# Optimization experiments

Hardware: AMD Instinct MI355X
Metric: run time of the kernel (lower is better)

Reference implementation:

```python
import jax, jax.numpy as jnp
import numpy as np

V, DM, DEPTH, N = 50257, 512, 8, 16  # vocab, dim, depth, ssm_dim
B, L = 2, 1024
GATE = 0.5  # fixed_gate=True blend


def layer_norm(x, g, b):
    mu = x.mean(-1, keepdims=True)
    xm = x - mu
    var = (xm * xm).mean(-1, keepdims=True)
    return xm * jax.lax.rsqrt(var + 1e-5) * g + b


def ssm(u, W_dt, b_dt, W_B, W_C, A_log, D_p):
    # selective SSM: h_t = exp(dt_t*A)*h_{t-1} + dt_t*B_t*u_t ; y_t = C_t.h_t + D*u_t
    dt = jax.nn.softplus(u @ W_dt + b_dt)            # (B,L,DM)
    Bm = u @ W_B                                      # (B,L,N)
    Cm = u @ W_C                                      # (B,L,N)
    A = -jnp.exp(A_log)                               # (DM,N), stable (negative)

    def step(h, inp):
        dt_t, B_t, C_t, u_t = inp                     # (B,DM),(B,N),(B,N),(B,DM)
        h = jnp.exp(dt_t[..., None] * A) * h + (dt_t * u_t)[..., None] * B_t[:, None, :]
        y = jnp.einsum('bdn,bn->bd', h, C_t)
        return h, y

    h0 = jnp.zeros((u.shape[0], DM, N), u.dtype)
    xs = (dt.transpose(1, 0, 2), Bm.transpose(1, 0, 2), Cm.transpose(1, 0, 2), u.transpose(1, 0, 2))
    _, ys = jax.lax.scan(step, h0, xs)
    return ys.transpose(1, 0, 2) + D_p * u


def wkv(x, W_r, W_k, W_v, W_o, t_decay, t_first):
    # RWKV-4 channel-wise WKV recurrence
    r = jax.nn.sigmoid(x @ W_r)
    k = jnp.clip(x @ W_k, -30.0, 30.0)
    v = x @ W_v
    w = jnp.exp(-jnp.exp(t_decay))                    # (DM,) decay in (0,1)

    def step(carry, inp):
        a, b = carry
        k_t, v_t = inp
        ek = jnp.exp(k_t)
        eu = jnp.exp(t_first + k_t)
        out = (a + eu * v_t) / (b + eu + 1e-6)
        return (w * a + ek * v_t, w * b + ek), out

    a0 = jnp.zeros((x.shape[0], DM), x.dtype)
    _, o = jax.lax.scan(step, (a0, jnp.zeros_like(a0)), (k.transpose(1, 0, 2), v.transpose(1, 0, 2)))
    return (r * o.transpose(1, 0, 2)) @ W_o


def setup_inputs() -> dict:
    key = jax.random.key(0)
    ks = jax.random.split(key, 16)
    s = 0.02
    inp = {
        'input_ids': jax.random.randint(ks[0], (B, L), 0, V, dtype=jnp.int32),
        'emb': jax.random.normal(ks[1], (V, DM), jnp.float32) * s,
        'ln1_g': jnp.ones((DEPTH, DM), jnp.float32),
        'ln1_b': jnp.zeros((DEPTH, DM), jnp.float32),
        'W_dt': jax.random.normal(ks[2], (DEPTH, DM, DM), jnp.float32) * s,
        'b_dt': jnp.zeros((DEPTH, DM), jnp.float32),
        'W_B': jax.random.normal(ks[3], (DEPTH, DM, N), jnp.float32) * s,
        'W_C': jax.random.normal(ks[4], (DEPTH, DM, N), jnp.float32) * s,
        'A_log': jnp.broadcast_to(jnp.log(jnp.arange(1, N + 1, dtype=jnp.float32)), (DEPTH, DM, N)).copy(),
        'D_p': jnp.ones((DEPTH, DM), jnp.float32),
        'ln2_g': jnp.ones((DEPTH, DM), jnp.float32),
        'ln2_b': jnp.zeros((DEPTH, DM), jnp.float32),
        'W_r': jax.random.normal(ks[5], (DEPTH, DM, DM), jnp.float32) * s,
        'W_k': jax.random.normal(ks[6], (DEPTH, DM, DM), jnp.float32) * s,
        'W_v': jax.random.normal(ks[7], (DEPTH, DM, DM), jnp.float32) * s,
        'W_o': jax.random.normal(ks[8], (DEPTH, DM, DM), jnp.float32) * s,
        't_decay': jax.random.normal(ks[9], (DEPTH, DM), jnp.float32) * 0.5,
        't_first': jax.random.normal(ks[10], (DEPTH, DM), jnp.float32) * 0.5,
        'lnf_g': jnp.ones((DM,), jnp.float32),
        'lnf_b': jnp.zeros((DM,), jnp.float32),
    }
    return inp


def reference(input_ids, emb, ln1_g, ln1_b, W_dt, b_dt, W_B, W_C, A_log, D_p,
              ln2_g, ln2_b, W_r, W_k, W_v, W_o, t_decay, t_first, lnf_g, lnf_b):
    x = emb[input_ids]                                # (B,L,DM)
    for i in range(DEPTH):
        x = x + GATE * ssm(layer_norm(x, ln1_g[i], ln1_b[i]),
                           W_dt[i], b_dt[i], W_B[i], W_C[i], A_log[i], D_p[i])
        x = x + GATE * wkv(layer_norm(x, ln2_g[i], ln2_b[i]),
                           W_r[i], W_k[i], W_v[i], W_o[i], t_decay[i], t_first[i])
    x = layer_norm(x, lnf_g, lnf_b)
    logits = x @ emb.T                                # tied LM head, (B,L,V)
    return logits
```

## Files before the change

kernel.cpp:

```cpp
#include <hip/hip_runtime.h>

#define DM 512
#define NST 16
#define NDEPTH 8
#define NB 2
#define NL 1024
#define MROWS 2048
#define VOCAB 50257
#define VPAD  50304
#define NCH 32
#define CLEN 32

typedef __attribute__((ext_vector_type(8))) short bf16x8;
typedef __attribute__((ext_vector_type(4))) float f32x4;
typedef __attribute__((ext_vector_type(8))) unsigned short ushort8;

#define AS1(p) ((const __attribute__((address_space(1))) void*)(p))
#define AS3(p) ((__attribute__((address_space(3))) void*)(p))

static __device__ __forceinline__ unsigned short f2bf(float f) {
  unsigned int x = __float_as_uint(f);
  unsigned int r = (x + 0x7FFFu + ((x >> 16) & 1u)) >> 16;
  return (unsigned short)r;
}
static __device__ __forceinline__ float bf2f(unsigned short u) {
  return __uint_as_float((unsigned int)u << 16);
}

__global__ __launch_bounds__(256) void k_gather(const int* __restrict__ ids,
    const float* __restrict__ emb, float* __restrict__ x)
{
  int gid = blockIdx.x * 256 + threadIdx.x;
  int row = gid >> 7, c = (gid & 127) * 4;
  int id = ids[row];
  *(float4*)(x + (size_t)row * DM + c) = *(const float4*)(emb + (size_t)id * DM + c);
}

__global__ void k_transpose(const float* __restrict__ Wdt, const float* __restrict__ Wr,
    const float* __restrict__ Wk, const float* __restrict__ Wv, const float* __restrict__ Wo,
    unsigned short* __restrict__ Tdtbc, unsigned short* __restrict__ Trkv, unsigned short* __restrict__ To)
{
  __shared__ float tile[32][33];
  int z = blockIdx.z, layer = z / 5, f = z % 5;
  const float* src;
  unsigned short* dst;
  size_t lw = (size_t)layer * DM * DM;
  if (f == 0)      { src = Wdt + lw; dst = Tdtbc + (size_t)layer * 640 * DM; }
  else if (f == 1) { src = Wr  + lw; dst = Trkv + (size_t)layer * 3 * DM * DM; }
  else if (f == 2) { src = Wk  + lw; dst = Trkv + (size_t)layer * 3 * DM * DM + DM * DM; }
  else if (f == 3) { src = Wv  + lw; dst = Trkv + (size_t)layer * 3 * DM * DM + 2 * DM * DM; }
  else             { src = Wo  + lw; dst = To   + lw; }
  int tx = threadIdx.x, ty = threadIdx.y;
  int kb = blockIdx.y * 32, nb = blockIdx.x * 32;
  #pragma unroll
  for (int i = 0; i < 4; i++)
    tile[ty + i * 8][tx] = src[(size_t)(kb + ty + i * 8) * DM + nb + tx];
  __syncthreads();
  #pragma unroll
  for (int i = 0; i < 4; i++)
    dst[(size_t)(nb + ty + i * 8) * DM + kb + tx] = f2bf(tile[tx][ty + i * 8]);
}

__global__ __launch_bounds__(256) void k_bcpack(const float* __restrict__ WB,
    const float* __restrict__ WC, unsigned short* __restrict__ Tdtbc)
{
  int gid = blockIdx.x * 256 + threadIdx.x;
  int k = gid & 511, n = (gid >> 9) & 127, layer = gid >> 16;
  float v = 0.f;
  if (n < 16)      v = WB[((size_t)layer * DM + k) * NST + n];
  else if (n < 32) v = WC[((size_t)layer * DM + k) * NST + (n - 16)];
  Tdtbc[(size_t)layer * 640 * DM + (size_t)(512 + n) * DM + k] = f2bf(v);
}

__global__ __launch_bounds__(256) void k_embcvt(const float* __restrict__ emb,
    unsigned short* __restrict__ out)
{
  int gid = blockIdx.x * 256 + threadIdx.x;
  size_t base = (size_t)gid * 8;
  int row = (int)(base >> 9);
  ushort8 o;
  if (row < VOCAB) {
    float4 a = *(const float4*)(emb + base);
    float4 b = *(const float4*)(emb + base + 4);
    o[0]=f2bf(a.x); o[1]=f2bf(a.y); o[2]=f2bf(a.z); o[3]=f2bf(a.w);
    o[4]=f2bf(b.x); o[5]=f2bf(b.y); o[6]=f2bf(b.z); o[7]=f2bf(b.w);
  } else {
    o = (ushort8)0;
  }
  *(ushort8*)(out + base) = o;
}

__global__ __launch_bounds__(256) void k_ln(const float* __restrict__ x,
    const float* __restrict__ g, const float* __restrict__ bb,
    float* __restrict__ of, unsigned short* __restrict__ ob)
{
  const int w = threadIdx.x >> 6, l = threadIdx.x & 63;
  const int row = blockIdx.x * 4 + w;
  const float* xr = x + (size_t)row * DM + l * 8;
  float4 v0 = *(const float4*)(xr);
  float4 v1 = *(const float4*)(xr + 4);
  float s = v0.x + v0.y + v0.z + v0.w + v1.x + v1.y + v1.z + v1.w;
  float q = v0.x*v0.x + v0.y*v0.y + v0.z*v0.z + v0.w*v0.w
          + v1.x*v1.x + v1.y*v1.y + v1.z*v1.z + v1.w*v1.w;
  #pragma unroll
  for (int m = 1; m < 64; m <<= 1) { s += __shfl_xor(s, m); q += __shfl_xor(q, m); }
  const float mu = s * (1.0f / DM);
  const float var = q * (1.0f / DM) - mu * mu;
  const float rs = rsqrtf(var + 1e-5f);
  const float4 g0 = *(const float4*)(g + l * 8);
  const float4 g1 = *(const float4*)(g + l * 8 + 4);
  const float4 b0 = *(const float4*)(bb + l * 8);
  const float4 b1 = *(const float4*)(bb + l * 8 + 4);
  float y[8];
  y[0] = (v0.x - mu) * rs * g0.x + b0.x;
  y[1] = (v0.y - mu) * rs * g0.y + b0.y;
  y[2] = (v0.z - mu) * rs * g0.z + b0.z;
  y[3] = (v0.w - mu) * rs * g0.w + b0.w;
  y[4] = (v1.x - mu) * rs * g1.x + b1.x;
  y[5] = (v1.y - mu) * rs * g1.y + b1.y;
  y[6] = (v1.z - mu) * rs * g1.z + b1.z;
  y[7] = (v1.w - mu) * rs * g1.w + b1.w;
  if (of) {
    float4 o0 = {y[0], y[1], y[2], y[3]}, o1 = {y[4], y[5], y[6], y[7]};
    *(float4*)(of + (size_t)row * DM + l * 8) = o0;
    *(float4*)(of + (size_t)row * DM + l * 8 + 4) = o1;
  }
  if (ob) {
    ushort8 o;
    #pragma unroll
    for (int j = 0; j < 8; j++) o[j] = f2bf(y[j]);
    *(ushort8*)(ob + (size_t)row * DM + l * 8) = o;
  }
}

template<int BM, int BN, int EPI>
__global__ __launch_bounds__(256) void gemm_bt(const unsigned short* __restrict__ A,
    const unsigned short* __restrict__ Bt, float* __restrict__ C, int N, int ldc,
    const float* __restrict__ bias, float* __restrict__ C2)
{
  constexpr int K = DM;
  constexpr int MI = BM / 32, NI = BN / 32;
  __shared__ unsigned short lsA[BM * 64];
  __shared__ unsigned short lsB[BN * 64];
  const int t = threadIdx.x;
  const int w = t >> 6, l = t & 63;
  const int wm = (w >> 1) * (BM / 2), wn = (w & 1) * (BN / 2);
  const size_t bm = (size_t)blockIdx.x * BM, bn = (size_t)blockIdx.y * BN;
  f32x4 acc[MI][NI] = {};
  const int srow = t >> 3, sslot = t & 7;
  const int gs = sslot ^ (srow & 7);
  const unsigned short* Ag = A + (bm + srow) * K + gs * 8;
  const unsigned short* Bg = Bt + (bn + srow) * K + gs * 8;
  const int lr = l & 15, lq = l >> 4;
  for (int k0 = 0; k0 < K; k0 += 64) {
    #pragma unroll
    for (int o = 0; o < BM / 32; ++o)
      __builtin_amdgcn_global_load_lds(AS1(Ag + (size_t)(o * 32) * K + k0),
          AS3(lsA + (o * 32 + srow) * 64 + sslot * 8), 16, 0, 0);
    #pragma unroll
    for (int o = 0; o < BN / 32; ++o)
      __builtin_amdgcn_global_load_lds(AS1(Bg + (size_t)(o * 32) * K + k0),
          AS3(lsB + (o * 32 + srow) * 64 + sslot * 8), 16, 0, 0);
    asm volatile("s_waitcnt vmcnt(0)" ::: "memory");
    __syncthreads();
    bf16x8 af[MI][2], bfr[NI][2];
    #pragma unroll
    for (int i = 0; i < MI; ++i) {
      int row = wm + i * 16 + lr;
      #pragma unroll
      for (int h = 0; h < 2; ++h)
        af[i][h] = *(const bf16x8*)(lsA + row * 64 + (((h * 4 + lq) ^ (row & 7)) * 8));
    }
    #pragma unroll
    for (int i = 0; i < NI; ++i) {
      int row = wn + i * 16 + lr;
      #pragma unroll
      for (int h = 0; h < 2; ++h)
        bfr[i][h] = *(const bf16x8*)(lsB + row * 64 + (((h * 4 + lq) ^ (row & 7)) * 8));
    }
    #pragma unroll
    for (int h = 0; h < 2; ++h)
      #pragma unroll
      for (int mi = 0; mi < MI; ++mi)
        #pragma unroll
        for (int ni = 0; ni < NI; ++ni)
          acc[mi][ni] = __builtin_amdgcn_mfma_f32_16x16x32_bf16(af[mi][h], bfr[ni][h], acc[mi][ni], 0, 0, 0);
    __syncthreads();
  }
  const int lg = l >> 4;
  #pragma unroll
  for (int mi = 0; mi < MI; ++mi) {
    #pragma unroll
    for (int ni = 0; ni < NI; ++ni) {
      int n = (int)bn + wn + ni * 16 + lr;
      size_t m0 = bm + wm + mi * 16 + lg * 4;
      #pragma unroll
      for (int j = 0; j < 4; ++j) {
        float v = acc[mi][ni][j];
        if (EPI == 0) {
          C[(m0 + j) * (size_t)ldc + n] = v;
        } else if (EPI == 2) {
          C2[(m0 + j) * (size_t)ldc + n] += 0.5f * v;
        } else {
          if (n < 512) {
            float b = v + bias[n];
            C[(m0 + j) * (size_t)512 + n] = fmaxf(b, 0.f) + log1pf(__expf(-fabsf(b)));
          } else if (n < 544) {
            C2[(m0 + j) * (size_t)32 + (n - 512)] = v;
          }
        }
      }
    }
  }
}

__global__ __launch_bounds__(512) void gemm_head(const unsigned short* __restrict__ A,
    const unsigned short* __restrict__ Bt, float* __restrict__ C)
{
  __shared__ unsigned short lsA[256 * 64];
  __shared__ unsigned short lsB[128 * 64];
  const int t = threadIdx.x;
  const int w = t >> 6, l = t & 63;
  const int wm = (w >> 1) * 64, wn = (w & 1) * 64;
  const int c = (int)blockIdx.x & 7, j = (int)blockIdx.x >> 3;
  const int ntile = c * 50 + (j >> 3), mtile = j & 7;
  if (ntile >= 393) return;
  const size_t bm = (size_t)mtile * 256, bn = (size_t)ntile * 128;
  f32x4 acc[4][4] = {};
  const int srow = t >> 3, sslot = t & 7;
  const int gs = sslot ^ (srow & 7);
  const unsigned short* Ag = A + (bm + srow) * DM + gs * 8;
  const unsigned short* Bg = Bt + (bn + srow) * DM + gs * 8;
  const int lr = l & 15, lq = l >> 4;
  for (int k0 = 0; k0 < DM; k0 += 64) {
    #pragma unroll
    for (int o = 0; o < 4; ++o)
      __builtin_amdgcn_global_load_lds(AS1(Ag + (size_t)(o * 64) * DM + k0),
          AS3(lsA + (o * 64 + srow) * 64 + sslot * 8), 16, 0, 0);
    #pragma unroll
    for (int o = 0; o < 2; ++o)
      __builtin_amdgcn_global_load_lds(AS1(Bg + (size_t)(o * 64) * DM + k0),
          AS3(lsB + (o * 64 + srow) * 64 + sslot * 8), 16, 0, 0);
    asm volatile("s_waitcnt vmcnt(0)" ::: "memory");
    __syncthreads();
    bf16x8 af[4][2], bfr[4][2];
    #pragma unroll
    for (int i = 0; i < 4; ++i) {
      int row = wm + i * 16 + lr;
      #pragma unroll
      for (int h = 0; h < 2; ++h)
        af[i][h] = *(const bf16x8*)(lsA + row * 64 + (((h * 4 + lq) ^ (row & 7)) * 8));
    }
    #pragma unroll
    for (int i = 0; i < 4; ++i) {
      int row = wn + i * 16 + lr;
      #pragma unroll
      for (int h = 0; h < 2; ++h)
        bfr[i][h] = *(const bf16x8*)(lsB + row * 64 + (((h * 4 + lq) ^ (row & 7)) * 8));
    }
    #pragma unroll
    for (int h = 0; h < 2; ++h)
      #pragma unroll
      for (int mi = 0; mi < 4; ++mi)
        #pragma unroll
        for (int ni = 0; ni < 4; ++ni)
          acc[mi][ni] = __builtin_amdgcn_mfma_f32_16x16x32_bf16(af[mi][h], bfr[ni][h], acc[mi][ni], 0, 0, 0);
    __syncthreads();
  }
  const int lg = l >> 4;
  #pragma unroll
  for (int mi = 0; mi < 4; ++mi) {
    #pragma unroll
    for (int ni = 0; ni < 4; ++ni) {
      int n = (int)bn + wn + ni * 16 + lr;
      if (n >= VOCAB) continue;
      size_t m0 = bm + wm + mi * 16 + lg * 4;
      #pragma unroll
      for (int jj = 0; jj < 4; ++jj)
        C[(m0 + jj) * (size_t)VOCAB + n] = acc[mi][ni][jj];
    }
  }
}

__global__ __launch_bounds__(256) void k_ssm1(const float* __restrict__ dt,
    const unsigned short* __restrict__ u, const float* __restrict__ BC,
    const float* __restrict__ A_log, float* __restrict__ Pb, float* __restrict__ Sb)
{
  const int t = threadIdx.x;
  const int grp = t >> 4, n = t & 15;
  const int cg = blockIdx.x & 63, ck = blockIdx.x >> 6;
  const int ch = cg * 16 + grp;
  const int b = ch >> 9, d = ch & 511;
  const float A = -__expf(A_log[d * NST + n]);
  const int t0 = ck * CLEN;
  const float* dtp = dt + ((size_t)b * NL + t0) * DM + d;
  const unsigned short* up = u + ((size_t)b * NL + t0) * DM + d;
  const float* bcp = BC + ((size_t)b * NL + t0) * 32 + n;
  float P = 1.f, S = 0.f;
  #pragma unroll
  for (int tt = 0; tt < CLEN; ++tt) {
    float dtv = dtp[(size_t)tt * DM];
    float uv  = bf2f(up[(size_t)tt * DM]);
    float Bv  = bcp[(size_t)tt * 32];
    float e = __expf(dtv * A);
    S = fmaf(e, S, dtv * uv * Bv);
    P *= e;
  }
  size_t cn = (size_t)ch * NST + n;
  Pb[cn * NCH + ck] = P;
  Sb[cn * NCH + ck] = S;
}

__global__ __launch_bounds__(256) void k_ssm2(const float* __restrict__ Pb,
    const float* __restrict__ Sb, float* __restrict__ H0)
{
  const int wid = blockIdx.x * 8 + (threadIdx.x >> 5);
  const int lane = threadIdx.x & 31;
  float coef = Pb[(size_t)wid * NCH + lane];
  float sum  = Sb[(size_t)wid * NCH + lane];
  #pragma unroll
  for (int m = 1; m < 32; m <<= 1) {
    float cr = __shfl_up(coef, m, 32);
    float sr = __shfl_up(sum, m, 32);
    if (lane >= m) { sum = fmaf(coef, sr, sum); coef *= cr; }
  }
  float hp = __shfl_up(sum, 1, 32);
  H0[(size_t)wid * NCH + lane] = (lane == 0) ? 0.f : hp;
}

__global__ __launch_bounds__(256) void k_ssm3(const float* __restrict__ dt,
    const unsigned short* __restrict__ u, const float* __restrict__ BC,
    const float* __restrict__ A_log, const float* __restrict__ Dp,
    const float* __restrict__ H0, float* __restrict__ x)
{
  const int t = threadIdx.x;
  const int grp = t >> 4, n = t & 15;
  const int cg = blockIdx.x & 63, ck = blockIdx.x >> 6;
  const int ch = cg * 16 + grp;
  const int b = ch >> 9, d = ch & 511;
  const float A = -__expf(A_log[d * NST + n]);
  const float Dpv = Dp[d];
  const int t0 = ck * CLEN;
  const float* dtp = dt + ((size_t)b * NL + t0) * DM + d;
  const unsigned short* up = u + ((size_t)b * NL + t0) * DM + d;
  const float* bcp = BC + ((size_t)b * NL + t0) * 32 + n;
  float* xp = x + ((size_t)b * NL + t0) * DM + d;
  size_t cn = (size_t)ch * NST + n;
  float h = H0[cn * NCH + ck];
  #pragma unroll
  for (int tt = 0; tt < CLEN; ++tt) {
    float dtv = dtp[(size_t)tt * DM];
    float uv  = bf2f(up[(size_t)tt * DM]);
    float Bv  = bcp[(size_t)tt * 32];
    float Cv  = bcp[(size_t)tt * 32 + 16];
    float e = __expf(dtv * A);
    h = fmaf(e, h, dtv * uv * Bv);
    float p2 = h * Cv;
    p2 += __shfl_xor(p2, 1);
    p2 += __shfl_xor(p2, 2);
    p2 += __shfl_xor(p2, 4);
    p2 += __shfl_xor(p2, 8);
    if (n == 0) xp[(size_t)tt * DM] += 0.5f * (p2 + Dpv * uv);
  }
}

__global__ __launch_bounds__(256) void k_wkv1(const float* __restrict__ rkv,
    const float* __restrict__ tdec, float* __restrict__ SaB, float* __restrict__ SbB)
{
  const int gid = blockIdx.x * 256 + threadIdx.x;
  const int ch = gid & 1023, ck = gid >> 10;
  const int b = ch >> 9, d = ch & 511;
  const float w = __expf(-__expf(tdec[d]));
  const float* base = rkv + ((size_t)b * NL + ck * CLEN) * 1536;
  float Sa = 0.f, Sb = 0.f;
  #pragma unroll
  for (int tt = 0; tt < CLEN; ++tt) {
    const float* row = base + (size_t)tt * 1536;
    float kt = row[512 + d];
    kt = fminf(30.f, fmaxf(-30.f, kt));
    float vt = row[1024 + d];
    float ek = __expf(kt);
    Sa = fmaf(w, Sa, ek * vt);
    Sb = fmaf(w, Sb, ek);
  }
  SaB[(size_t)ch * NCH + ck] = Sa;
  SbB[(size_t)ch * NCH + ck] = Sb;
}

__global__ __launch_bounds__(256) void k_wkv2(const float* __restrict__ SaB,
    const float* __restrict__ SbB, const float* __restrict__ tdec,
    float* __restrict__ HaB, float* __restrict__ HbB)
{
  const int ch = blockIdx.x * 8 + (threadIdx.x >> 5);
  const int lane = threadIdx.x & 31;
  const int d = ch & 511;
  float coef = __expf(-32.f * __expf(tdec[d]));
  float sa = SaB[(size_t)ch * NCH + lane];
  float sb = SbB[(size_t)ch * NCH + lane];
  #pragma unroll
  for (int m = 1; m < 32; m <<= 1) {
    float cr  = __shfl_up(coef, m, 32);
    float sar = __shfl_up(sa, m, 32);
    float sbr = __shfl_up(sb, m, 32);
    if (lane >= m) { sa = fmaf(coef, sar, sa); sb = fmaf(coef, sbr, sb); coef *= cr; }
  }
  float ha = __shfl_up(sa, 1, 32);
  float hb = __shfl_up(sb, 1, 32);
  HaB[(size_t)ch * NCH + lane] = (lane == 0) ? 0.f : ha;
  HbB[(size_t)ch * NCH + lane] = (lane == 0) ? 0.f : hb;
}

__global__ __launch_bounds__(256) void k_wkv3(const float* __restrict__ rkv,
    const float* __restrict__ tdec, const float* __restrict__ tfir,
    const float* __restrict__ HaB, const float* __restrict__ HbB,
    unsigned short* __restrict__ ro)
{
  const int gid = blockIdx.x * 256 + threadIdx.x;
  const int ch = gid & 1023, ck = gid >> 10;
  const int b = ch >> 9, d = ch & 511;
  const float w = __expf(-__expf(tdec[d]));
  const float tf = tfir[d];
  float a = HaB[(size_t)ch * NCH + ck];
  float bden = HbB[(size_t)ch * NCH + ck];
  const int t0 = ck * CLEN;
  const float* base = rkv + ((size_t)b * NL + t0) * 1536;
  unsigned short* rop = ro + ((size_t)b * NL + t0) * DM + d;
  #pragma unroll
  for (int tt = 0; tt < CLEN; ++tt) {
    const float* row = base + (size_t)tt * 1536;
    float rv = row[d];
    float kt = row[512 + d];
    kt = fminf(30.f, fmaxf(-30.f, kt));
    float vt = row[1024 + d];
    float ek = __expf(kt);
    float eu = __expf(tf + kt);
    float out = __fdividef(a + eu * vt, bden + eu + 1e-6f);
    float sig = __fdividef(1.f, 1.f + __expf(-rv));
    rop[(size_t)tt * DM] = f2bf(sig * out);
    a = fmaf(w, a, ek * vt);
    bden = fmaf(w, bden, ek);
  }
}

extern "C" void kernel_launch(void* const* d_in, const int* in_sizes, int n_in,
                              void* d_out, int out_size, void* d_ws, size_t ws_size,
                              hipStream_t stream)
{
  const int*   ids   = (const int*)d_in[0];
  const float* emb   = (const float*)d_in[1];
  const float* ln1_g = (const float*)d_in[2];
  const float* ln1_b = (const float*)d_in[3];
  const float* W_dt  = (const float*)d_in[4];
  const float* b_dt  = (const float*)d_in[5];
  const float* W_B   = (const float*)d_in[6];
  const float* W_C   = (const float*)d_in[7];
  const float* A_log = (const float*)d_in[8];
  const float* D_p   = (const float*)d_in[9];
  const float* ln2_g = (const float*)d_in[10];
  const float* ln2_b = (const float*)d_in[11];
  const float* W_r   = (const float*)d_in[12];
  const float* W_k   = (const float*)d_in[13];
  const float* W_v   = (const float*)d_in[14];
  const float* W_o   = (const float*)d_in[15];
  const float* t_dec = (const float*)d_in[16];
  const float* t_fir = (const float*)d_in[17];
  const float* lnf_g = (const float*)d_in[18];
  const float* lnf_b = (const float*)d_in[19];

  char* p = (char*)d_ws;
  float*          xres  = (float*)(p + 0);
  float*          dtb   = (float*)(p + 8388608);
  float*          rkv   = (float*)(p + 12582912);
  float*          BCb   = (float*)(p + 25165824);
  unsigned short* abuf  = (unsigned short*)(p + 25427968);
  unsigned short* Tdtbc = (unsigned short*)(p + 27525120);
  unsigned short* To    = (unsigned short*)(p + 32768000);
  unsigned short* Trkv  = (unsigned short*)(p + 36962304);
  unsigned short* Tem   = (unsigned short*)(p + 49545216);

  float* Pb  = rkv;
  float* Sb  = rkv + 524288;
  float* H0  = rkv + 1048576;
  float* SaB = dtb;
  float* SbB = dtb + 32768;
  float* HaB = dtb + 65536;
  float* HbB = dtb + 98304;

  k_gather<<<1024, 256, 0, stream>>>(ids, emb, xres);
  k_transpose<<<dim3(16, 16, 40), dim3(32, 8), 0, stream>>>(W_dt, W_r, W_k, W_v, W_o, Tdtbc, Trkv, To);
  k_bcpack<<<2048, 256, 0, stream>>>(W_B, W_C, Tdtbc);
  k_embcvt<<<12576, 256, 0, stream>>>(emb, Tem);

  for (int i = 0; i < NDEPTH; ++i) {
    k_ln<<<512, 256, 0, stream>>>(xres, ln1_g + i * DM, ln1_b + i * DM, nullptr, abuf);
    gemm_bt<64, 128, 3><<<dim3(32, 5), 256, 0, stream>>>(abuf,
        Tdtbc + (size_t)i * 640 * DM, dtb, 640, 512, b_dt + i * DM, BCb);
    k_ssm1<<<2048, 256, 0, stream>>>(dtb, abuf, BCb, A_log + (size_t)i * DM * NST, Pb, Sb);
    k_ssm2<<<2048, 256, 0, stream>>>(Pb, Sb, H0);
    k_ssm3<<<2048, 256, 0, stream>>>(dtb, abuf, BCb, A_log + (size_t)i * DM * NST,
        D_p + i * DM, H0, xres);
    k_ln<<<512, 256, 0, stream>>>(xres, ln2_g + i * DM, ln2_b + i * DM, nullptr, abuf);
    gemm_bt<64, 128, 0><<<dim3(32, 12), 256, 0, stream>>>(abuf,
        Trkv + (size_t)i * 3 * DM * DM, rkv, 1536, 1536, nullptr, nullptr);
    k_wkv1<<<128, 256, 0, stream>>>(rkv, t_dec + i * DM, SaB, SbB);
    k_wkv2<<<128, 256, 0, stream>>>(SaB, SbB, t_dec + i * DM, HaB, HbB);
    k_wkv3<<<128, 256, 0, stream>>>(rkv, t_dec + i * DM, t_fir + i * DM, HaB, HbB, abuf);
    gemm_bt<64, 128, 2><<<dim3(32, 4), 256, 0, stream>>>(abuf,
        To + (size_t)i * DM * DM, nullptr, 512, 512, nullptr, xres);
  }

  k_ln<<<512, 256, 0, stream>>>(xres, lnf_g, lnf_b, nullptr, abuf);
  gemm_head<<<3200, 512, 0, stream>>>(abuf, Tem, (float*)d_out);
}
```

Before: 1.124 ms.

## Fuse three-phase SSM and WKV chunked scans into cooperative kernels with grid sync

Merges the three SSM scan kernels (chunk reduce, cross-chunk prefix, chunk apply) into one cooperative kernel, and does the same for the three WKV kernels. Phases are separated by grid-wide barriers instead of separate kernel launches. The SSM kernel runs on 1024 blocks, each handling two virtual blocks, so the whole grid can be resident at once. This removes launch gaps and per-launch overhead, at the cost of grid-sync latency and the residency constraint a cooperative launch imposes.

After: 3.606 ms. +220.7%, slower.

```diff
diff --git a/kernel.cpp b/kernel.cpp
--- a/kernel.cpp
+++ b/kernel.cpp
@@ -1,4 +1,7 @@
 #include <hip/hip_runtime.h>
+#include <hip/hip_cooperative_groups.h>
+
+namespace cg = cooperative_groups;
 
 #define DM 512
 #define NST 16
@@ -282,163 +285,158 @@
   }
 }
 
-__global__ __launch_bounds__(256) void k_ssm1(const float* __restrict__ dt,
+__global__ __launch_bounds__(256, 4) void k_ssm_all(const float* __restrict__ dt,
     const unsigned short* __restrict__ u, const float* __restrict__ BC,
-    const float* __restrict__ A_log, float* __restrict__ Pb, float* __restrict__ Sb)
-{
+    const float* __restrict__ A_log, const float* __restrict__ Dp,
+    float* __restrict__ Pb, float* __restrict__ Sb, float* __restrict__ H0,
+    float* __restrict__ x)
+{
+  cg::grid_group gridg = cg::this_grid();
   const int t = threadIdx.x;
   const int grp = t >> 4, n = t & 15;
-  const int cg = blockIdx.x & 63, ck = blockIdx.x >> 6;
-  const int ch = cg * 16 + grp;
-  const int b = ch >> 9, d = ch & 511;
-  const float A = -__expf(A_log[d * NST + n]);
-  const int t0 = ck * CLEN;
-  const float* dtp = dt + ((size_t)b * NL + t0) * DM + d;
-  const unsigned short* up = u + ((size_t)b * NL + t0) * DM + d;
-  const float* bcp = BC + ((size_t)b * NL + t0) * 32 + n;
-  float P = 1.f, S = 0.f;
-  #pragma unroll
-  for (int tt = 0; tt < CLEN; ++tt) {
-    float dtv = dtp[(size_t)tt * DM];
-    float uv  = bf2f(up[(size_t)tt * DM]);
-    float Bv  = bcp[(size_t)tt * 32];
-    float e = __expf(dtv * A);
-    S = fmaf(e, S, dtv * uv * Bv);
-    P *= e;
-  }
-  size_t cn = (size_t)ch * NST + n;
-  Pb[cn * NCH + ck] = P;
-  Sb[cn * NCH + ck] = S;
-}
-
-__global__ __launch_bounds__(256) void k_ssm2(const float* __restrict__ Pb,
-    const float* __restrict__ Sb, float* __restrict__ H0)
-{
-  const int wid = blockIdx.x * 8 + (threadIdx.x >> 5);
-  const int lane = threadIdx.x & 31;
-  float coef = Pb[(size_t)wid * NCH + lane];
-  float sum  = Sb[(size_t)wid * NCH + lane];
-  #pragma unroll
-  for (int m = 1; m < 32; m <<= 1) {
-    float cr = __shfl_up(coef, m, 32);
-    float sr = __shfl_up(sum, m, 32);
-    if (lane >= m) { sum = fmaf(coef, sr, sum); coef *= cr; }
-  }
-  float hp = __shfl_up(sum, 1, 32);
-  H0[(size_t)wid * NCH + lane] = (lane == 0) ? 0.f : hp;
-}
-
-__global__ __launch_bounds__(256) void k_ssm3(const float* __restrict__ dt,
-    const unsigned short* __restrict__ u, const float* __restrict__ BC,
-    const float* __restrict__ A_log, const float* __restrict__ Dp,
-    const float* __restrict__ H0, float* __restrict__ x)
-{
-  const int t = threadIdx.x;
-  const int grp = t >> 4, n = t & 15;
-  const int cg = blockIdx.x & 63, ck = blockIdx.x >> 6;
-  const int ch = cg * 16 + grp;
-  const int b = ch >> 9, d = ch & 511;
-  const float A = -__expf(A_log[d * NST + n]);
-  const float Dpv = Dp[d];
-  const int t0 = ck * CLEN;
-  const float* dtp = dt + ((size_t)b * NL + t0) * DM + d;
-  const unsigned short* up = u + ((size_t)b * NL + t0) * DM + d;
-  const float* bcp = BC + ((size_t)b * NL + t0) * 32 + n;
-  float* xp = x + ((size_t)b * NL + t0) * DM + d;
-  size_t cn = (size_t)ch * NST + n;
-  float h = H0[cn * NCH + ck];
-  #pragma unroll
-  for (int tt = 0; tt < CLEN; ++tt) {
-    float dtv = dtp[(size_t)tt * DM];
-    float uv  = bf2f(up[(size_t)tt * DM]);
-    float Bv  = bcp[(size_t)tt * 32];
-    float Cv  = bcp[(size_t)tt * 32 + 16];
-    float e = __expf(dtv * A);
-    h = fmaf(e, h, dtv * uv * Bv);
-    float p2 = h * Cv;
-    p2 += __shfl_xor(p2, 1);
-    p2 += __shfl_xor(p2, 2);
-    p2 += __shfl_xor(p2, 4);
-    p2 += __shfl_xor(p2, 8);
-    if (n == 0) xp[(size_t)tt * DM] += 0.5f * (p2 + Dpv * uv);
-  }
-}
-
-__global__ __launch_bounds__(256) void k_wkv1(const float* __restrict__ rkv,
-    const float* __restrict__ tdec, float* __restrict__ SaB, float* __restrict__ SbB)
-{
+  for (int it = 0; it < 2; ++it) {
+    const int vb = (int)blockIdx.x * 2 + it;
+    const int cgi = vb & 63, ck = vb >> 6;
+    const int ch = cgi * 16 + grp;
+    const int b = ch >> 9, d = ch & 511;
+    const float A = -__expf(A_log[d * NST + n]);
+    const int t0 = ck * CLEN;
+    const float* dtp = dt + ((size_t)b * NL + t0) * DM + d;
+    const unsigned short* up = u + ((size_t)b * NL + t0) * DM + d;
+    const float* bcp = BC + ((size_t)b * NL + t0) * 32 + n;
+    float P = 1.f, S = 0.f;
+    #pragma unroll
+    for (int tt = 0; tt < CLEN; ++tt) {
+      float dtv = dtp[(size_t)tt * DM];
+      float uv  = bf2f(up[(size_t)tt * DM]);
+      float Bv  = bcp[(size_t)tt * 32];
+      float e = __expf(dtv * A);
+      S = fmaf(e, S, dtv * uv * Bv);
+      P *= e;
+    }
+    size_t cn = (size_t)ch * NST + n;
+    Pb[cn * NCH + ck] = P;
+    Sb[cn * NCH + ck] = S;
+  }
+  gridg.sync();
+  for (int it = 0; it < 2; ++it) {
+    const int vb = (int)blockIdx.x * 2 + it;
+    const int wid = vb * 8 + (t >> 5);
+    const int lane = t & 31;
+    float coef = Pb[(size_t)wid * NCH + lane];
+    float sum  = Sb[(size_t)wid * NCH + lane];
+    #pragma unroll
+    for (int m = 1; m < 32; m <<= 1) {
+      float cr = __shfl_up(coef, m, 32);
+      float sr = __shfl_up(sum, m, 32);
+      if (lane >= m) { sum = fmaf(coef, sr, sum); coef *= cr; }
+    }
+    float hp = __shfl_up(sum, 1, 32);
+    H0[(size_t)wid * NCH + lane] = (lane == 0) ? 0.f : hp;
+  }
+  gridg.sync();
+  for (int it = 0; it < 2; ++it) {
+    const int vb = (int)blockIdx.x * 2 + it;
+    const int cgi = vb & 63, ck = vb >> 6;
+    const int ch = cgi * 16 + grp;
+    const int b = ch >> 9, d = ch & 511;
+    const float A = -__expf(A_log[d * NST + n]);
+    const float Dpv = Dp[d];
+    const int t0 = ck * CLEN;
+    const float* dtp = dt + ((size_t)b * NL + t0) * DM + d;
+    const unsigned short* up = u + ((size_t)b * NL + t0) * DM + d;
+    const float* bcp = BC + ((size_t)b * NL + t0) * 32 + n;
+    float* xp = x + ((size_t)b * NL + t0) * DM + d;
+    size_t cn = (size_t)ch * NST + n;
+    float h = H0[cn * NCH + ck];
+    #pragma unroll
+    for (int tt = 0; tt < CLEN; ++tt) {
+      float dtv = dtp[(size_t)tt * DM];
+      float uv  = bf2f(up[(size_t)tt * DM]);
+      float Bv  = bcp[(size_t)tt * 32];
+      float Cv  = bcp[(size_t)tt * 32 + 16];
+      float e = __expf(dtv * A);
+      h = fmaf(e, h, dtv * uv * Bv);
+      float p2 = h * Cv;
+      p2 += __shfl_xor(p2, 1);
+      p2 += __shfl_xor(p2, 2);
+      p2 += __shfl_xor(p2, 4);
+      p2 += __shfl_xor(p2, 8);
+      if (n == 0) xp[(size_t)tt * DM] += 0.5f * (p2 + Dpv * uv);
+    }
+  }
+}
+
+__global__ __launch_bounds__(256, 4) void k_wkv_all(const float* __restrict__ rkv,
+    const float* __restrict__ tdec, const float* __restrict__ tfir,
+    float* __restrict__ SaB, float* __restrict__ SbB,
+    float* __restrict__ HaB, float* __restrict__ HbB,
+    unsigned short* __restrict__ ro)
+{
+  cg::grid_group gridg = cg::this_grid();
   const int gid = blockIdx.x * 256 + threadIdx.x;
   const int ch = gid & 1023, ck = gid >> 10;
   const int b = ch >> 9, d = ch & 511;
   const float w = __expf(-__expf(tdec[d]));
-  const float* base = rkv + ((size_t)b * NL + ck * CLEN) * 1536;
-  float Sa = 0.f, Sb = 0.f;
-  #pragma unroll
-  for (int tt = 0; tt < CLEN; ++tt) {
-    const float* row = base + (size_t)tt * 1536;
-    float kt = row[512 + d];
-    kt = fminf(30.f, fmaxf(-30.f, kt));
-    float vt = row[1024 + d];
-    float ek = __expf(kt);
-    Sa = fmaf(w, Sa, ek * vt);
-    Sb = fmaf(w, Sb, ek);
-  }
-  SaB[(size_t)ch * NCH + ck] = Sa;
-  SbB[(size_t)ch * NCH + ck] = Sb;
-}
-
-__global__ __launch_bounds__(256) void k_wkv2(const float* __restrict__ SaB,
-    const float* __restrict__ SbB, const float* __restrict__ tdec,
-    float* __restrict__ HaB, float* __restrict__ HbB)
-{
-  const int ch = blockIdx.x * 8 + (threadIdx.x >> 5);
-  const int lane = threadIdx.x & 31;
-  const int d = ch & 511;
-  float coef = __expf(-32.f * __expf(tdec[d]));
-  float sa = SaB[(size_t)ch * NCH + lane];
-  float sb = SbB[(size_t)ch * NCH + lane];
-  #pragma unroll
-  for (int m = 1; m < 32; m <<= 1) {
-    float cr  = __shfl_up(coef, m, 32);
-    float sar = __shfl_up(sa, m, 32);
-    float sbr = __shfl_up(sb, m, 32);
-    if (lane >= m) { sa = fmaf(coef, sar, sa); sb = fmaf(coef, sbr, sb); coef *= cr; }
-  }
-  float ha = __shfl_up(sa, 1, 32);
-  float hb = __shfl_up(sb, 1, 32);
-  HaB[(size_t)ch * NCH + lane] = (lane == 0) ? 0.f : ha;
-  HbB[(size_t)ch * NCH + lane] = (lane == 0) ? 0.f : hb;
-}
-
-__global__ __launch_bounds__(256) void k_wkv3(const float* __restrict__ rkv,
-    const float* __restrict__ tdec, const float* __restrict__ tfir,
-    const float* __restrict__ HaB, const float* __restrict__ HbB,
-    unsigned short* __restrict__ ro)
-{
-  const int gid = blockIdx.x * 256 + threadIdx.x;
-  const int ch = gid & 1023, ck = gid >> 10;
-  const int b = ch >> 9, d = ch & 511;
-  const float w = __expf(-__expf(tdec[d]));
-  const float tf = tfir[d];
-  float a = HaB[(size_t)ch * NCH + ck];
-  float bden = HbB[(size_t)ch * NCH + ck];
-  const int t0 = ck * CLEN;
-  const float* base = rkv + ((size_t)b * NL + t0) * 1536;
-  unsigned short* rop = ro + ((size_t)b * NL + t0) * DM + d;
-  #pragma unroll
-  for (int tt = 0; tt < CLEN; ++tt) {
-    const float* row = base + (size_t)tt * 1536;
-    float rv = row[d];
-    float kt = row[512 + d];
-    kt = fminf(30.f, fmaxf(-30.f, kt));
-    float vt = row[1024 + d];
-    float ek = __expf(kt);
-    float eu = __expf(tf + kt);
-    float out = __fdividef(a + eu * vt, bden + eu + 1e-6f);
-    float sig = __fdividef(1.f, 1.f + __expf(-rv));
-    rop[(size_t)tt * DM] = f2bf(sig * out);
-    a = fmaf(w, a, ek * vt);
-    bden = fmaf(w, bden, ek);
+  {
+    const float* base = rkv + ((size_t)b * NL + ck * CLEN) * 1536;
+    float Sa = 0.f, Sb = 0.f;
+    #pragma unroll
+    for (int tt = 0; tt < CLEN; ++tt) {
+      const float* row = base + (size_t)tt * 1536;
+      float kt = row[512 + d];
+      kt = fminf(30.f, fmaxf(-30.f, kt));
+      float vt = row[1024 + d];
+      float ek = __expf(kt);
+      Sa = fmaf(w, Sa, ek * vt);
+      Sb = fmaf(w, Sb, ek);
+    }
+    SaB[(size_t)ch * NCH + ck] = Sa;
+    SbB[(size_t)ch * NCH + ck] = Sb;
+  }
+  gridg.sync();
+  {
+    const int ch2 = blockIdx.x * 8 + (threadIdx.x >> 5);
+    const int lane = threadIdx.x & 31;
+    const int d2 = ch2 & 511;
+    float coef = __expf(-32.f * __expf(tdec[d2]));
+    float sa = SaB[(size_t)ch2 * NCH + lane];
+    float sb = SbB[(size_t)ch2 * NCH + lane];
+    #pragma unroll
+    for (int m = 1; m < 32; m <<= 1) {
+      float cr  = __shfl_up(coef, m, 32);
+      float sar = __shfl_up(sa, m, 32);
+      float sbr = __shfl_up(sb, m, 32);
+      if (lane >= m) { sa = fmaf(coef, sar, sa); sb = fmaf(coef, sbr, sb); coef *= cr; }
+    }
+    float ha = __shfl_up(sa, 1, 32);
+    float hb = __shfl_up(sb, 1, 32);
+    HaB[(size_t)ch2 * NCH + lane] = (lane == 0) ? 0.f : ha;
+    HbB[(size_t)ch2 * NCH + lane] = (lane == 0) ? 0.f : hb;
+  }
+  gridg.sync();
+  {
+    const float tf = tfir[d];
+    float a = HaB[(size_t)ch * NCH + ck];
+    float bden = HbB[(size_t)ch * NCH + ck];
+    const int t0 = ck * CLEN;
+    const float* base = rkv + ((size_t)b * NL + t0) * 1536;
+    unsigned short* rop = ro + ((size_t)b * NL + t0) * DM + d;
+    #pragma unroll
+    for (int tt = 0; tt < CLEN; ++tt) {
+      const float* row = base + (size_t)tt * 1536;
+      float rv = row[d];
+      float kt = row[512 + d];
+      kt = fminf(30.f, fmaxf(-30.f, kt));
+      float vt = row[1024 + d];
+      float ek = __expf(kt);
+      float eu = __expf(tf + kt);
+      float out = __fdividef(a + eu * vt, bden + eu + 1e-6f);
+      float sig = __fdividef(1.f, 1.f + __expf(-rv));
+      rop[(size_t)tt * DM] = f2bf(sig * out);
+      a = fmaf(w, a, ek * vt);
+      bden = fmaf(w, bden, ek);
+    }
   }
 }
 
@@ -495,16 +493,23 @@
     k_ln<<<512, 256, 0, stream>>>(xres, ln1_g + i * DM, ln1_b + i * DM, nullptr, abuf);
     gemm_bt<64, 128, 3><<<dim3(32, 5), 256, 0, stream>>>(abuf,
         Tdtbc + (size_t)i * 640 * DM, dtb, 640, 512, b_dt + i * DM, BCb);
-    k_ssm1<<<2048, 256, 0, stream>>>(dtb, abuf, BCb, A_log + (size_t)i * DM * NST, Pb, Sb);
-    k_ssm2<<<2048, 256, 0, stream>>>(Pb, Sb, H0);
-    k_ssm3<<<2048, 256, 0, stream>>>(dtb, abuf, BCb, A_log + (size_t)i * DM * NST,
-        D_p + i * DM, H0, xres);
+    {
+      const float* dtc = dtb; const unsigned short* uc = abuf; const float* bcc = BCb;
+      const float* al = A_log + (size_t)i * DM * NST; const float* dp = D_p + i * DM;
+      float* pb = Pb; float* sb = Sb; float* h0 = H0; float* xr = xres;
+      void* args[] = {&dtc, &uc, &bcc, &al, &dp, &pb, &sb, &h0, &xr};
+      hipLaunchCooperativeKernel((void*)k_ssm_all, dim3(1024), dim3(256), args, 0, stream);
+    }
     k_ln<<<512, 256, 0, stream>>>(xres, ln2_g + i * DM, ln2_b + i * DM, nullptr, abuf);
     gemm_bt<64, 128, 0><<<dim3(32, 12), 256, 0, stream>>>(abuf,
         Trkv + (size_t)i * 3 * DM * DM, rkv, 1536, 1536, nullptr, nullptr);
-    k_wkv1<<<128, 256, 0, stream>>>(rkv, t_dec + i * DM, SaB, SbB);
-    k_wkv2<<<128, 256, 0, stream>>>(SaB, SbB, t_dec + i * DM, HaB, HbB);
-    k_wkv3<<<128, 256, 0, stream>>>(rkv, t_dec + i * DM, t_fir + i * DM, HaB, HbB, abuf);
+    {
+      const float* rk = rkv; const float* td = t_dec + i * DM; const float* tf = t_fir + i * DM;
+      float* sa = SaB; float* sb2 = SbB; float* hA = HaB; float* hB = HbB;
+      unsigned short* ro = abuf;
+      void* args[] = {&rk, &td, &tf, &sa, &sb2, &hA, &hB, &ro};
+      hipLaunchCooperativeKernel((void*)k_wkv_all, dim3(128), dim3(256), args, 0, stream);
+    }
     gemm_bt<64, 128, 2><<<dim3(32, 4), 256, 0, stream>>>(abuf,
         To + (size_t)i * DM * DM, nullptr, 512, 512, nullptr, xres);
   }
```
